# Kernel tuning notes

Hardware: AMD Instinct MI355X
Metric: run time of the kernel (lower is better)

Reference implementation:

```python
import jax, jax.numpy as jnp
import numpy as np

B, S, IN_DIM, OUT_DIM = 4, 2048, 1024, 1024
NEG = -9e15

def _xavier(key, shape, gain=1.414):
    fan_in, fan_out = shape[0], shape[1]
    a = gain * np.sqrt(6.0 / (fan_in + fan_out))
    return jax.random.uniform(key, shape, jnp.float32, -a, a)

def setup_inputs() -> dict:
    key = jax.random.key(0)
    ks = jax.random.split(key, 8)
    x = jax.random.normal(ks[0], (B, S, IN_DIM), jnp.float32)
    W_query = _xavier(ks[1], (IN_DIM, OUT_DIM))
    W_key = _xavier(ks[2], (IN_DIM, OUT_DIM))
    W_value = _xavier(ks[3], (IN_DIM, OUT_DIM))
    # torch Linear default init (kaiming-uniform-ish); values don't matter for correctness baseline
    W1 = _xavier(ks[4], (OUT_DIM + IN_DIM, OUT_DIM), gain=1.0)
    b1 = jnp.zeros((OUT_DIM,), jnp.float32)
    W2 = _xavier(ks[5], (OUT_DIM, OUT_DIM), gain=1.0)
    b2 = jnp.zeros((OUT_DIM,), jnp.float32)
    return {"x": x, "W_query": W_query, "W_key": W_key, "W_value": W_value,
            "W1": W1, "b1": b1, "W2": W2, "b2": b2}

def reference(x, W_query, W_key, W_value, W1, b1, W2, b2):
    # QKV projections: [B,S,in] @ [in,out] -> [B,S,out]
    q = jnp.einsum('bsi,io->bso', x, W_query)
    k = jnp.einsum('bsi,io->bso', x, W_key)
    v = jnp.einsum('bsi,io->bso', x, W_value)
    scale = 1.0 / jnp.sqrt(jnp.float32(OUT_DIM))
    e = jnp.einsum('bqd,bkd->bqk', q, k) * scale  # [B,S,S]
    causal = jnp.tril(jnp.ones((S, S), jnp.float32))  # mask > 0 keeps lower triangle
    attn = jnp.where(causal > 0, e, jnp.float32(NEG))
    attn = jax.nn.softmax(attn, axis=2)
    # dropout: eval mode (train=False) -> identity
    out = jnp.einsum('bqk,bkd->bqd', attn, v)  # [B,S,out]
    h = jnp.concatenate([out, x], axis=-1)  # [B,S,out+in]
    h = jax.nn.relu(jnp.einsum('bsf,fo->bso', h, W1) + b1)
    return jnp.einsum('bsf,fo->bso', h, W2) + b2
```

## Files before the change

kernel.cpp:

```cpp
#include <hip/hip_runtime.h>
#include <stdint.h>

typedef __attribute__((ext_vector_type(8))) short short8;
typedef __attribute__((ext_vector_type(4))) float f32x4;

__device__ __forceinline__ unsigned short f32_to_bf16(float f) {
    unsigned int u = __float_as_uint(f);
    u += 0x7FFFu + ((u >> 16) & 1u);
    return (unsigned short)(u >> 16);
}
__device__ __forceinline__ float bf16_to_f32(unsigned short h) {
    return __uint_as_float((unsigned int)h << 16);
}

__device__ __forceinline__ short8 load8_f32_as_bf16(const float* __restrict__ ap) {
    f32x4 f0 = *(const f32x4*)ap;
    f32x4 f1 = *(const f32x4*)(ap + 4);
    union { short8 s; unsigned short u[8]; } cv;
#pragma unroll
    for (int t = 0; t < 4; ++t) {
        cv.u[t]     = f32_to_bf16(f0[t]);
        cv.u[t + 4] = f32_to_bf16(f1[t]);
    }
    return cv.s;
}

__device__ __forceinline__ void gld_lds16(const void* g, void* l) {
    __builtin_amdgcn_global_load_lds(
        (const __attribute__((address_space(1))) unsigned int*)(unsigned long long)(uintptr_t)g,
        (__attribute__((address_space(3))) unsigned int*)(unsigned int)(uintptr_t)l,
        16, 0, 0);
}

template<int AMODE, int EPI, int SWIZ, bool KLIMIT>
__global__ __launch_bounds__(256, 4)
void gemm128(const unsigned short* __restrict__ A, const unsigned short* __restrict__ A2,
             int lda, int lda2, int ksplit,
             const unsigned short* __restrict__ B, int ldb,
             void* __restrict__ C, int ldc, int K,
             long aStride, long bStride, long cStride,
             const float* __restrict__ bias, long biasStride, float scale)
{
    int mblk, nblk;
    if (SWIZ == 1) {
        int lin = blockIdx.y * gridDim.x + blockIdx.x;
        int mchunk = gridDim.y >> 3;
        int xcd = lin & 7, idx = lin >> 3;
        mblk = xcd * mchunk + idx % mchunk;
        nblk = idx / mchunk;
    } else if (SWIZ == 2) {
        int x = blockIdx.x;
        int a = (int)((sqrtf(8.f * x + 1.f) - 1.f) * 0.5f);
        while ((a + 1) * (a + 2) / 2 <= x) ++a;
        while (a * (a + 1) / 2 > x) --a;
        mblk = a;
        nblk = x - a * (a + 1) / 2;
    } else {
        mblk = blockIdx.y;
        nblk = blockIdx.x;
    }
    int m0 = mblk * 128;
    int n0 = nblk * 128;

    int z = blockIdx.z;
    const unsigned short* Ab = A + (size_t)z * aStride;
    const unsigned short* Bb = B + (size_t)z * bStride;

    __shared__ __align__(16) short As[128 * 64];
    __shared__ __align__(16) short Bs[128 * 64];

    int tid  = threadIdx.x;
    int lane = tid & 63, wid = tid >> 6;
    int wm = (wid & 1) * 64, wn = (wid >> 1) * 64;
    int fr = lane & 15, fq = lane >> 4;
    int sw0 = ((fq    ) ^ (fr & 7)) * 16;
    int sw1 = ((fq ^ 4) ^ (fr & 7)) * 16;

    int rS = tid >> 3;
    int cS = ((tid & 7) ^ (rS & 7)) * 8;
    char* AsB = (char*)As; char* BsB = (char*)Bs;

    int kend = KLIMIT ? min(K, m0 + 128) : K;

    f32x4 acc[4][4];
#pragma unroll
    for (int i = 0; i < 4; ++i)
#pragma unroll
    for (int j = 0; j < 4; ++j) acc[i][j] = f32x4{0.f, 0.f, 0.f, 0.f};

    for (int k0 = 0; k0 < kend; k0 += 64) {
        const unsigned short* Asrc = Ab;
        int koff = k0, ldax = lda;
        if (AMODE == 2 && k0 >= ksplit) { Asrc = A2; koff = k0 - ksplit; ldax = lda2; }
        const unsigned short* pa = Asrc + (size_t)(m0 + rS) * ldax + koff + cS;
        const unsigned short* pb = Bb   + (size_t)(n0 + rS) * ldb  + k0   + cS;
#pragma unroll
        for (int t = 0; t < 4; ++t) {
            gld_lds16(pa + (size_t)(32 * t) * ldax, AsB + t * 4096 + tid * 16);
            gld_lds16(pb + (size_t)(32 * t) * ldb,  BsB + t * 4096 + tid * 16);
        }
        __syncthreads();

#pragma unroll
        for (int kh = 0; kh < 2; ++kh) {
            int sw = kh ? sw1 : sw0;
            short8 a[4], b[4];
#pragma unroll
            for (int i = 0; i < 4; ++i) {
                a[i] = *(const short8*)(AsB + (wm + i * 16 + fr) * 128 + sw);
                b[i] = *(const short8*)(BsB + (wn + i * 16 + fr) * 128 + sw);
            }
#pragma unroll
            for (int i = 0; i < 4; ++i)
#pragma unroll
            for (int j = 0; j < 4; ++j)
                acc[i][j] = __builtin_amdgcn_mfma_f32_16x16x32_bf16(a[i], b[j], acc[i][j], 0, 0, 0);
        }
        __syncthreads();
    }

    if (EPI == 6) {
        unsigned short* Cz = (unsigned short*)C + (size_t)z * cStride;
        float* rs = const_cast<float*>(bias) + z * biasStride;
#pragma unroll
        for (int i = 0; i < 4; ++i)
#pragma unroll
        for (int r = 0; r < 4; ++r) {
            int row = m0 + wm + i * 16 + fq * 4 + r;
            float s = 0.f;
#pragma unroll
            for (int j = 0; j < 4; ++j) {
                int col = n0 + wn + j * 16 + fr;
                float e = (col <= row) ? __expf(acc[i][j][r] * scale - 16.f) : 0.f;
                s += e;
                Cz[(size_t)row * ldc + col] = f32_to_bf16(e);
            }
            s += __shfl_xor(s, 1);
            s += __shfl_xor(s, 2);
            s += __shfl_xor(s, 4);
            s += __shfl_xor(s, 8);
            if (fr == 0) atomicAdd(&rs[row], s);
        }
    } else if (EPI == 4) {
        unsigned short* Cz = (unsigned short*)C + (size_t)z * cStride;
#pragma unroll
        for (int i = 0; i < 4; ++i)
#pragma unroll
        for (int r = 0; r < 4; ++r) {
            int row = m0 + wm + i * 16 + fq * 4 + r;
            float inv = 1.f / bias[z * biasStride + row];
#pragma unroll
            for (int j = 0; j < 4; ++j) {
                int col = n0 + wn + j * 16 + fr;
                Cz[(size_t)row * ldc + col] = f32_to_bf16(acc[i][j][r] * inv);
            }
        }
    } else {
#pragma unroll
        for (int i = 0; i < 4; ++i)
#pragma unroll
        for (int j = 0; j < 4; ++j)
#pragma unroll
        for (int r = 0; r < 4; ++r) {
            int row = m0 + wm + i * 16 + fq * 4 + r;
            int col = n0 + wn + j * 16 + fr;
            float v = acc[i][j][r];
            if (EPI == 0) {
                ((unsigned short*)C + (size_t)z * cStride)[(size_t)row * ldc + col] = f32_to_bf16(v);
            } else if (EPI == 2) {
                v += bias[col];
                v = v > 0.f ? v : 0.f;
                ((unsigned short*)C + (size_t)z * cStride)[(size_t)row * ldc + col] = f32_to_bf16(v);
            } else {
                ((float*)C + (size_t)z * cStride)[(size_t)row * ldc + col] = v + bias[col];
            }
        }
    }
}

__global__ __launch_bounds__(256)
void f32_to_bf16_vec(const float* __restrict__ in, unsigned short* __restrict__ out)
{
    size_t i = ((size_t)blockIdx.x * 256 + threadIdx.x) * 8;
    *(short8*)(out + i) = load8_f32_as_bf16(in + i);
}

__global__ __launch_bounds__(256)
void transpose_qkv_w(const float* __restrict__ Wq, const float* __restrict__ Wk,
                     const float* __restrict__ Wv, unsigned short* __restrict__ WT)
{
    int z = blockIdx.z;
    const float* in = z == 0 ? Wq : (z == 1 ? Wk : Wv);
    unsigned short* out = WT + (size_t)z * 1024 * 1024;
    __shared__ float t[32][33];
    int tx = threadIdx.x, ty = threadIdx.y;
    int r0 = blockIdx.y * 32, c0 = blockIdx.x * 32;
    for (int i = ty; i < 32; i += 8)
        t[i][tx] = in[(size_t)(r0 + i) * 1024 + c0 + tx];
    __syncthreads();
    for (int i = ty; i < 32; i += 8)
        out[(size_t)(c0 + i) * 1024 + r0 + tx] = f32_to_bf16(t[tx][i]);
}

__global__ __launch_bounds__(256)
void transpose_f32_bf16(const float* __restrict__ in, unsigned short* __restrict__ out,
                        int rows, int cols)
{
    __shared__ float t[32][33];
    int tx = threadIdx.x, ty = threadIdx.y;
    int r0 = blockIdx.y * 32, c0 = blockIdx.x * 32;
    for (int i = ty; i < 32; i += 8)
        t[i][tx] = in[(size_t)(r0 + i) * cols + c0 + tx];
    __syncthreads();
    for (int i = ty; i < 32; i += 8)
        out[(size_t)(c0 + i) * rows + r0 + tx] = f32_to_bf16(t[tx][i]);
}

__global__ __launch_bounds__(256)
void transpose_v_kernel(const unsigned short* __restrict__ v, unsigned short* __restrict__ vT)
{
    int b = blockIdx.z;
    const unsigned short* in = v + (size_t)b * 2048 * 1024;
    unsigned short* out = vT + (size_t)b * 1024 * 2048;
    __shared__ unsigned short t[64][65];
    int tx = threadIdx.x, ty = threadIdx.y;
    int r0 = blockIdx.y * 64, c0 = blockIdx.x * 64;
    for (int i = ty; i < 64; i += 4)
        t[i][tx] = in[(size_t)(r0 + i) * 1024 + c0 + tx];
    __syncthreads();
    for (int i = ty; i < 64; i += 4)
        out[(size_t)(c0 + i) * 2048 + r0 + tx] = t[tx][i];
}

extern "C" void kernel_launch(void* const* d_in, const int* in_sizes, int n_in,
                              void* d_out, int out_size, void* d_ws, size_t ws_size,
                              hipStream_t stream)
{
    const float* x  = (const float*)d_in[0];
    const float* Wq = (const float*)d_in[1];
    const float* Wk = (const float*)d_in[2];
    const float* Wv = (const float*)d_in[3];
    const float* W1 = (const float*)d_in[4];
    const float* b1 = (const float*)d_in[5];
    const float* W2 = (const float*)d_in[6];
    const float* b2 = (const float*)d_in[7];
    float* out = (float*)d_out;

    size_t off = 0;
    auto alloc = [&](size_t bytes) {
        char* r = (char*)d_ws + off;
        off += (bytes + 255) & ~(size_t)255;
        return r;
    };
    const size_t TOK = (size_t)8192 * 1024;
    unsigned short* WT   = (unsigned short*)alloc((size_t)3072 * 1024 * 2);
    unsigned short* W1T  = (unsigned short*)alloc((size_t)1024 * 2048 * 2);
    unsigned short* W2T  = (unsigned short*)alloc((size_t)1024 * 1024 * 2);
    unsigned short* xb   = (unsigned short*)alloc(TOK * 2);
    unsigned short* vT   = (unsigned short*)alloc((size_t)4 * 1024 * 2048 * 2);
    unsigned short* attn = (unsigned short*)alloc(TOK * 2);
    float*          rsum = (float*)         alloc((size_t)4 * 2048 * 4);
    unsigned short* q    = (unsigned short*)alloc(TOK * 2 * 2 + (size_t)4 * 2048 * 2048 * 2);
    unsigned short* k    = q + TOK;
    unsigned short* v    = k + TOK;
    unsigned short* S    = v;
    unsigned short* h1   = S;

    hipMemsetAsync(rsum, 0, (size_t)4 * 2048 * 4, stream);

    dim3 tb(32, 8);
    transpose_qkv_w<<<dim3(32, 32, 3), tb, 0, stream>>>(Wq, Wk, Wv, WT);
    transpose_f32_bf16<<<dim3(32, 64), tb, 0, stream>>>(W1, W1T, 2048, 1024);
    transpose_f32_bf16<<<dim3(32, 32), tb, 0, stream>>>(W2, W2T, 1024, 1024);
    f32_to_bf16_vec<<<4096, 256, 0, stream>>>(x, xb);

    gemm128<0, 0, 1, false><<<dim3(8, 64, 3), 256, 0, stream>>>(
        xb, nullptr, 1024, 0, 0, WT, 1024, q, 1024, 1024,
        0, (long)1024 * 1024, (long)TOK, nullptr, 0, 0.f);

    transpose_v_kernel<<<dim3(16, 32, 4), dim3(64, 4), 0, stream>>>(v, vT);

    gemm128<0, 6, 2, false><<<dim3(136, 1, 4), 256, 0, stream>>>(
        q, nullptr, 1024, 0, 0, k, 1024, S, 2048, 1024,
        (long)2048 * 1024, (long)2048 * 1024, (long)2048 * 2048, rsum, 2048, 0.03125f);
    gemm128<0, 4, 0, true><<<dim3(8, 16, 4), 256, 0, stream>>>(
        S, nullptr, 2048, 0, 0, vT, 2048, attn, 1024, 2048,
        (long)2048 * 2048, (long)1024 * 2048, (long)2048 * 1024, rsum, 2048, 0.f);

    gemm128<2, 2, 1, false><<<dim3(8, 64, 1), 256, 0, stream>>>(
        attn, xb, 1024, 1024, 1024, W1T, 2048, h1, 1024, 2048, 0, 0, 0, b1, 0, 0.f);
    gemm128<0, 3, 1, false><<<dim3(8, 64, 1), 256, 0, stream>>>(
        h1, nullptr, 1024, 0, 0, W2T, 1024, out, 1024, 1024, 0, 0, 0, b2, 0, 0.f);
}
```

Before: 326.3 us.

## Compute V transposed directly via swapped GEMM, merge prep kernels, rebalance causal PV grid

Fuses the x conversion, weight transposes and rsum zeroing into one prep kernel, which removes several launches and the memset. V^T is now produced directly by a GEMM of Wv^T against x (with a new N-major XCD swizzle), so the separate V projection output and the transpose kernel go away. The PV GEMM gets a swizzle that reverses the row-block order for batches 2 and 3, to balance the triangular causal work across the grid. The cost is a different GEMM shape for V with an 8192 ldc, whose store pattern may be less efficient.

```diff
diff --git a/kernel.cpp b/kernel.cpp
--- a/kernel.cpp
+++ b/kernel.cpp
@@ -8,9 +8,6 @@
     unsigned int u = __float_as_uint(f);
     u += 0x7FFFu + ((u >> 16) & 1u);
     return (unsigned short)(u >> 16);
-}
-__device__ __forceinline__ float bf16_to_f32(unsigned short h) {
-    return __uint_as_float((unsigned int)h << 16);
 }
 
 __device__ __forceinline__ short8 load8_f32_as_bf16(const float* __restrict__ ap) {
@@ -41,6 +38,7 @@
              long aStride, long bStride, long cStride,
              const float* __restrict__ bias, long biasStride, float scale)
 {
+    int z = blockIdx.z;
     int mblk, nblk;
     if (SWIZ == 1) {
         int lin = blockIdx.y * gridDim.x + blockIdx.x;
@@ -55,6 +53,15 @@
         while (a * (a + 1) / 2 > x) --a;
         mblk = a;
         nblk = x - a * (a + 1) / 2;
+    } else if (SWIZ == 3) {
+        int lin = blockIdx.y * gridDim.x + blockIdx.x;
+        int nchunk = gridDim.x >> 3;
+        int xcd = lin & 7, idx = lin >> 3;
+        nblk = xcd * nchunk + idx % nchunk;
+        mblk = idx / nchunk;
+    } else if (SWIZ == 4) {
+        mblk = (z & 2) ? ((int)gridDim.y - 1 - (int)blockIdx.y) : blockIdx.y;
+        nblk = blockIdx.x;
     } else {
         mblk = blockIdx.y;
         nblk = blockIdx.x;
@@ -62,7 +69,6 @@
     int m0 = mblk * 128;
     int n0 = nblk * 128;
 
-    int z = blockIdx.z;
     const unsigned short* Ab = A + (size_t)z * aStride;
     const unsigned short* Bb = B + (size_t)z * bStride;
 
@@ -178,58 +184,55 @@
     }
 }
 
+__device__ __forceinline__ void transpose_tile32(const float* __restrict__ in,
+                                                 unsigned short* __restrict__ out,
+                                                 int rows, int cols, int bx, int by, int tid)
+{
+    __shared__ float t[32][33];
+    int tx = tid & 31, ty = tid >> 5;
+    int r0 = by * 32, c0 = bx * 32;
+#pragma unroll
+    for (int i = 0; i < 4; ++i)
+        t[ty + i * 8][tx] = in[(size_t)(r0 + ty + i * 8) * cols + c0 + tx];
+    __syncthreads();
+#pragma unroll
+    for (int i = 0; i < 4; ++i)
+        out[(size_t)(c0 + ty + i * 8) * rows + r0 + tx] = f32_to_bf16(t[tx][ty + i * 8]);
+}
+
 __global__ __launch_bounds__(256)
-void f32_to_bf16_vec(const float* __restrict__ in, unsigned short* __restrict__ out)
-{
-    size_t i = ((size_t)blockIdx.x * 256 + threadIdx.x) * 8;
-    *(short8*)(out + i) = load8_f32_as_bf16(in + i);
-}
-
-__global__ __launch_bounds__(256)
-void transpose_qkv_w(const float* __restrict__ Wq, const float* __restrict__ Wk,
-                     const float* __restrict__ Wv, unsigned short* __restrict__ WT)
-{
-    int z = blockIdx.z;
-    const float* in = z == 0 ? Wq : (z == 1 ? Wk : Wv);
-    unsigned short* out = WT + (size_t)z * 1024 * 1024;
-    __shared__ float t[32][33];
-    int tx = threadIdx.x, ty = threadIdx.y;
-    int r0 = blockIdx.y * 32, c0 = blockIdx.x * 32;
-    for (int i = ty; i < 32; i += 8)
-        t[i][tx] = in[(size_t)(r0 + i) * 1024 + c0 + tx];
-    __syncthreads();
-    for (int i = ty; i < 32; i += 8)
-        out[(size_t)(c0 + i) * 1024 + r0 + tx] = f32_to_bf16(t[tx][i]);
-}
-
-__global__ __launch_bounds__(256)
-void transpose_f32_bf16(const float* __restrict__ in, unsigned short* __restrict__ out,
-                        int rows, int cols)
-{
-    __shared__ float t[32][33];
-    int tx = threadIdx.x, ty = threadIdx.y;
-    int r0 = blockIdx.y * 32, c0 = blockIdx.x * 32;
-    for (int i = ty; i < 32; i += 8)
-        t[i][tx] = in[(size_t)(r0 + i) * cols + c0 + tx];
-    __syncthreads();
-    for (int i = ty; i < 32; i += 8)
-        out[(size_t)(c0 + i) * rows + r0 + tx] = f32_to_bf16(t[tx][i]);
-}
-
-__global__ __launch_bounds__(256)
-void transpose_v_kernel(const unsigned short* __restrict__ v, unsigned short* __restrict__ vT)
-{
-    int b = blockIdx.z;
-    const unsigned short* in = v + (size_t)b * 2048 * 1024;
-    unsigned short* out = vT + (size_t)b * 1024 * 2048;
-    __shared__ unsigned short t[64][65];
-    int tx = threadIdx.x, ty = threadIdx.y;
-    int r0 = blockIdx.y * 64, c0 = blockIdx.x * 64;
-    for (int i = ty; i < 64; i += 4)
-        t[i][tx] = in[(size_t)(r0 + i) * 1024 + c0 + tx];
-    __syncthreads();
-    for (int i = ty; i < 64; i += 4)
-        out[(size_t)(c0 + i) * 2048 + r0 + tx] = t[tx][i];
+void prep_kernel(const float* __restrict__ x,
+                 const float* __restrict__ Wq, const float* __restrict__ Wk,
+                 const float* __restrict__ Wv, const float* __restrict__ W1,
+                 const float* __restrict__ W2,
+                 unsigned short* __restrict__ xb, unsigned short* __restrict__ WT,
+                 unsigned short* __restrict__ W1T, unsigned short* __restrict__ W2T,
+                 float* __restrict__ rsum)
+{
+    int idx = blockIdx.x;
+    int tid = threadIdx.x;
+    if (idx < 4096) {
+        size_t i = ((size_t)idx * 256 + tid) * 8;
+        *(short8*)(xb + i) = load8_f32_as_bf16(x + i);
+    } else if (idx < 7168) {
+        int t = idx - 4096;
+        int w = t >> 10; t &= 1023;
+        const float* in = w == 0 ? Wq : (w == 1 ? Wk : Wv);
+        transpose_tile32(in, WT + (size_t)w * 1024 * 1024, 1024, 1024,
+                         t & 31, t >> 5, tid);
+    } else if (idx < 9216) {
+        int t = idx - 7168;
+        transpose_tile32(W1, W1T, 2048, 1024, t & 31, t >> 5, tid);
+    } else if (idx < 10240) {
+        int t = idx - 9216;
+        transpose_tile32(W2, W2T, 1024, 1024, t & 31, t >> 5, tid);
+    } else {
+        int t = idx - 10240;
+        f32x4 zero = {0.f, 0.f, 0.f, 0.f};
+        float* p = rsum + ((size_t)t * 256 + tid) * 8;
+        *(f32x4*)p = zero;
+        *(f32x4*)(p + 4) = zero;
+    }
 }
 
 extern "C" void kernel_launch(void* const* d_in, const int* in_sizes, int n_in,
@@ -257,35 +260,29 @@
     unsigned short* W1T  = (unsigned short*)alloc((size_t)1024 * 2048 * 2);
     unsigned short* W2T  = (unsigned short*)alloc((size_t)1024 * 1024 * 2);
     unsigned short* xb   = (unsigned short*)alloc(TOK * 2);
-    unsigned short* vT   = (unsigned short*)alloc((size_t)4 * 1024 * 2048 * 2);
+    unsigned short* vT   = (unsigned short*)alloc((size_t)1024 * 8192 * 2);
     unsigned short* attn = (unsigned short*)alloc(TOK * 2);
     float*          rsum = (float*)         alloc((size_t)4 * 2048 * 4);
-    unsigned short* q    = (unsigned short*)alloc(TOK * 2 * 2 + (size_t)4 * 2048 * 2048 * 2);
-    unsigned short* k    = q + TOK;
-    unsigned short* v    = k + TOK;
-    unsigned short* S    = v;
+    unsigned short* q    = (unsigned short*)alloc(TOK * 2);
+    unsigned short* k    = (unsigned short*)alloc(TOK * 2);
+    unsigned short* S    = (unsigned short*)alloc((size_t)4 * 2048 * 2048 * 2);
     unsigned short* h1   = S;
 
-    hipMemsetAsync(rsum, 0, (size_t)4 * 2048 * 4, stream);
-
-    dim3 tb(32, 8);
-    transpose_qkv_w<<<dim3(32, 32, 3), tb, 0, stream>>>(Wq, Wk, Wv, WT);
-    transpose_f32_bf16<<<dim3(32, 64), tb, 0, stream>>>(W1, W1T, 2048, 1024);
-    transpose_f32_bf16<<<dim3(32, 32), tb, 0, stream>>>(W2, W2T, 1024, 1024);
-    f32_to_bf16_vec<<<4096, 256, 0, stream>>>(x, xb);
-
-    gemm128<0, 0, 1, false><<<dim3(8, 64, 3), 256, 0, stream>>>(
+    prep_kernel<<<10244, 256, 0, stream>>>(x, Wq, Wk, Wv, W1, W2, xb, WT, W1T, W2T, rsum);
+
+    gemm128<0, 0, 1, false><<<dim3(8, 64, 2), 256, 0, stream>>>(
         xb, nullptr, 1024, 0, 0, WT, 1024, q, 1024, 1024,
         0, (long)1024 * 1024, (long)TOK, nullptr, 0, 0.f);
-
-    transpose_v_kernel<<<dim3(16, 32, 4), dim3(64, 4), 0, stream>>>(v, vT);
+    gemm128<0, 0, 3, false><<<dim3(64, 8, 1), 256, 0, stream>>>(
+        WT + (size_t)2 * 1024 * 1024, nullptr, 1024, 0, 0, xb, 1024, vT, 8192, 1024,
+        0, 0, 0, nullptr, 0, 0.f);
 
     gemm128<0, 6, 2, false><<<dim3(136, 1, 4), 256, 0, stream>>>(
         q, nullptr, 1024, 0, 0, k, 1024, S, 2048, 1024,
         (long)2048 * 1024, (long)2048 * 1024, (long)2048 * 2048, rsum, 2048, 0.03125f);
-    gemm128<0, 4, 0, true><<<dim3(8, 16, 4), 256, 0, stream>>>(
-        S, nullptr, 2048, 0, 0, vT, 2048, attn, 1024, 2048,
-        (long)2048 * 2048, (long)1024 * 2048, (long)2048 * 1024, rsum, 2048, 0.f);
+    gemm128<0, 4, 4, true><<<dim3(8, 16, 4), 256, 0, stream>>>(
+        S, nullptr, 2048, 0, 0, vT, 8192, attn, 1024, 2048,
+        (long)2048 * 2048, (long)2048, (long)2048 * 1024, rsum, 2048, 0.f);
 
     gemm128<2, 2, 1, false><<<dim3(8, 64, 1), 256, 0, stream>>>(
         attn, xb, 1024, 1024, 1024, W1T, 2048, h1, 1024, 2048, 0, 0, 0, b1, 0, 0.f);
```

After: 301.5 us. 1.08x faster.
